# Performance work log

Hardware: AMD Instinct MI355X
Metric: run time of the kernel (lower is better)

The kernel has to match this reference:

```python
import jax, jax.numpy as jnp
import numpy as np

N, M, D = 131072, 2048, 2


def setup_inputs() -> dict:
    key = jax.random.key(0)
    k1, k2 = jax.random.split(key)
    sample = jax.random.normal(k1, (N, D), dtype=jnp.float32)
    mu = jax.random.uniform(k2, (M, D), dtype=jnp.float32)
    # A initialized as 15 * I per component, exactly as in the torch module
    A = (15.0 * jnp.broadcast_to(jnp.eye(D, dtype=jnp.float32), (M, D, D))).astype(jnp.float32)
    w = jnp.ones((M, 1), dtype=jnp.float32)
    return {"sample": sample, "mu": mu, "A": A, "w": w}


def reference(sample, mu, A, w):
    """GaussianMixture.log_likelihoods(sample): logsumexp_j( wlog_j - (x-mu_j)^T G_j (x-mu_j) )."""
    # update_covariances: G_m = A_m A_m^T / 2, shape (M, D, D)
    G = jnp.einsum('mij,mkj->mik', A, A) * 0.5
    g00, g01, g10, g11 = G[:, 0, 0], G[:, 0, 1], G[:, 1, 0], G[:, 1, 1]  # (M,)
    # covariances_determinants (2x2 case) + weights_log
    dets = g00 * g11 - g01 * g10                                          # (M,)
    wlog = jax.nn.log_softmax(w, axis=0)[:, 0] + 0.5 * jnp.log(dets)      # (M,)
    # Pairwise Mahalanobis quadratic form, D=2 expanded to avoid an (N,M,D) temp
    dx0 = sample[:, 0:1] - mu[None, :, 0]   # (N, M)
    dx1 = sample[:, 1:2] - mu[None, :, 1]   # (N, M)
    q = g00 * dx0 * dx0 + (g01 + g10) * dx0 * dx1 + g11 * dx1 * dx1       # (N, M)
    # mode='lse' reduction of kernel_product: log sum_j exp(wlog_j - q_ij)
    ll = jax.nn.logsumexp(wlog[None, :] - q, axis=1, keepdims=True)       # (N, 1)
    return ll
```

## Files before the change

### kernel.cpp

```cpp
#include <hip/hip_runtime.h>
#include <math.h>


#if __has_builtin(__builtin_amdgcn_exp2f)
#define EXP2(x) __builtin_amdgcn_exp2f(x)
#else
#define EXP2(x) exp2f(x)
#endif

typedef float v2f __attribute__((ext_vector_type(2)));

#if __has_builtin(__builtin_elementwise_max)
#define PKMAX(a, b) __builtin_elementwise_max(a, b)
#else
static __device__ inline v2f PKMAX(v2f a, v2f b) {
  v2f r; r.x = fmaxf(a.x, b.x); r.y = fmaxf(a.y, b.y); return r;
}
#endif

#define SPLIT 4
#define YSPLIT 8
#define CH 16

__global__ __launch_bounds__(256) void prep_kernel(
    const float* __restrict__ mu,
    const float* __restrict__ A,
    const float* __restrict__ w,
    float* __restrict__ C,
    int M) {
  __shared__ float red[256];
  const int t = threadIdx.x;

  float mx = -INFINITY;
  for (int m = t; m < M; m += 256) mx = fmaxf(mx, w[m]);
  red[t] = mx; __syncthreads();
  for (int s = 128; s > 0; s >>= 1) {
    if (t < s) red[t] = fmaxf(red[t], red[t + s]);
    __syncthreads();
  }
  const float wmax = red[0]; __syncthreads();

  float sum = 0.f;
  for (int m = t; m < M; m += 256) sum += expf(w[m] - wmax);
  red[t] = sum; __syncthreads();
  for (int s = 128; s > 0; s >>= 1) {
    if (t < s) red[t] += red[t + s];
    __syncthreads();
  }
  const float logZ = wmax + logf(red[0]);

  const float LOG2E = 1.44269504088896340736f;
  const int Ms = M / gridDim.x;
  const int mlo = blockIdx.x * Ms, mhi = mlo + Ms;
  for (int m = mlo + t; m < mhi; m += 256) {
    const float a00 = A[m * 4 + 0], a01 = A[m * 4 + 1];
    const float a10 = A[m * 4 + 2], a11 = A[m * 4 + 3];
    const float g00 = 0.5f * (a00 * a00 + a01 * a01);
    const float g01 = 0.5f * (a00 * a10 + a01 * a11);
    const float g11 = 0.5f * (a10 * a10 + a11 * a11);
    const float g01s = 2.0f * g01;
    const float det = g00 * g11 - g01 * g01;
    const float wlog = (w[m] - logZ) + 0.5f * logf(det);
    const float mu0 = mu[m * 2 + 0], mu1 = mu[m * 2 + 1];
    const float c0 = wlog - (g00 * mu0 * mu0 + g01s * mu0 * mu1 + g11 * mu1 * mu1);
    const float c2 = 2.0f * g00 * mu0 + g01s * mu1;
    const float c4 = 2.0f * g11 * mu1 + g01s * mu0;
    C[0 * M + m] = LOG2E * c0;
    C[1 * M + m] = LOG2E * -g00;
    C[2 * M + m] = LOG2E * c2;
    C[3 * M + m] = LOG2E * -g11;
    C[4 * M + m] = LOG2E * c4;
    C[5 * M + m] = LOG2E * -g01s;
  }

  if (blockIdx.x == 0) {
    __shared__ int uni[256];
    const float r00 = A[0], r01 = A[1], r10 = A[2], r11 = A[3];
    const float rg00 = 0.5f * (r00 * r00 + r01 * r01);
    const float rg01 = 0.5f * (r00 * r10 + r01 * r11);
    const float rg11 = 0.5f * (r10 * r10 + r11 * r11);
    int myuni = 1;
    for (int m = t; m < M; m += 256) {
      const float a00 = A[m * 4 + 0], a01 = A[m * 4 + 1];
      const float a10 = A[m * 4 + 2], a11 = A[m * 4 + 3];
      const float g00 = 0.5f * (a00 * a00 + a01 * a01);
      const float g01 = 0.5f * (a00 * a10 + a01 * a11);
      const float g11 = 0.5f * (a10 * a10 + a11 * a11);
      myuni &= (g00 == rg00) & (g01 == rg01) & (g11 == rg11);
    }
    uni[t] = myuni; __syncthreads();
    for (int s = 128; s > 0; s >>= 1) {
      if (t < s) uni[t] &= uni[t + s];
      __syncthreads();
    }
    if (t == 0) {
      ((int*)C)[6 * M + 0] = uni[0];
      C[6 * M + 1] = LOG2E * -rg00;
      C[6 * M + 2] = LOG2E * -rg11;
      C[6 * M + 3] = LOG2E * -2.0f * rg01;
    }
  }
}

__global__ __launch_bounds__(256) void gmix_kernel(
    const float* __restrict__ sample,
    const float* __restrict__ C,
    float* __restrict__ P,
    int N, int M) {
  __shared__ float Lmx[SPLIT][2][64];
  __shared__ float Lsm[SPLIT][2][64];

  const int lane = threadIdx.x & 63;
  const int wave = __builtin_amdgcn_readfirstlane((int)(threadIdx.x >> 6));
  const int nA = blockIdx.x * 128 + lane;
  const int nB = nA + 64;

  const float2 xA = (nA < N) ? ((const float2*)sample)[nA] : make_float2(0.f, 0.f);
  const float2 xB = (nB < N) ? ((const float2*)sample)[nB] : make_float2(0.f, 0.f);
  const v2f x0p = {xA.x, xB.x};
  const v2f x1p = {xA.y, xB.y};

  const int flag = ((const int*)C)[6 * M + 0];
  const float cb1 = C[6 * M + 1];
  const float cb3 = C[6 * M + 2];
  const float cb5 = C[6 * M + 3];

  const int Mq = M / (SPLIT * YSPLIT);
  const int m0 = (blockIdx.y * SPLIT + wave) * Mq;
  const float* __restrict__ C0 = C + m0;
  const float* __restrict__ C1 = C + M + m0;
  const float* __restrict__ C2 = C + 2 * M + m0;
  const float* __restrict__ C3 = C + 3 * M + m0;
  const float* __restrict__ C4 = C + 4 * M + m0;
  const float* __restrict__ C5 = C + 5 * M + m0;

  v2f basep = {0.f, 0.f};
  float mxA = -INFINITY, sA = 0.0f;
  float mxB = -INFINITY, sB = 0.0f;

  if (flag) {
    basep = cb1 * x0p * x0p + cb3 * x1p * x1p + cb5 * x0p * x1p;
#pragma unroll
    for (int m = 0; m < 64; m += CH) {
      float c0r[CH], c2r[CH], c4r[CH];
#pragma unroll
      for (int j = 0; j < CH; ++j) {
        c0r[j] = C0[m + j]; c2r[j] = C2[m + j]; c4r[j] = C4[m + j];
      }
      v2f a[CH];
#pragma unroll
      for (int j = 0; j < CH; ++j) {
        v2f t = x0p * c2r[j] + c0r[j];
        a[j] = x1p * c4r[j] + t;
      }
      v2f cm01 = PKMAX(a[0], a[1]);
      v2f cm23 = PKMAX(a[2], a[3]);
      v2f cm45 = PKMAX(a[4], a[5]);
      v2f cm67 = PKMAX(a[6], a[7]);
#pragma unroll
      for (int j = 8; j < CH; j += 4) {
        cm01 = PKMAX(cm01, a[j]);
        cm23 = PKMAX(cm23, a[j + 1]);
        cm45 = PKMAX(cm45, a[j + 2]);
        cm67 = PKMAX(cm67, a[j + 3]);
      }
      const v2f cm = PKMAX(PKMAX(cm01, cm23), PKMAX(cm45, cm67));
      const float nmA = fmaxf(mxA, cm.x);
      const float nmB = fmaxf(mxB, cm.y);
      sA *= EXP2(mxA - nmA);
      sB *= EXP2(mxB - nmB);
      const v2f nmp = {nmA, nmB};
      float lA0 = 0.f, lA1 = 0.f, lB0 = 0.f, lB1 = 0.f;
#pragma unroll
      for (int j = 0; j < CH; j += 2) {
        const v2f d0 = a[j] - nmp;
        const v2f d1 = a[j + 1] - nmp;
        lA0 += EXP2(d0.x);
        lB0 += EXP2(d0.y);
        lA1 += EXP2(d1.x);
        lB1 += EXP2(d1.y);
      }
      sA += lA0 + lA1; mxA = nmA;
      sB += lB0 + lB1; mxB = nmB;
    }
  } else {
    for (int m = 0; m < Mq; m += CH) {
      v2f a[CH];
#pragma unroll
      for (int j = 0; j < CH; ++j) {
        const float c0 = C0[m + j], c1 = C1[m + j], c2 = C2[m + j];
        const float c3 = C3[m + j], c4 = C4[m + j], c5 = C5[m + j];
        v2f t0 = x0p * c1 + c2;
        t0 = x1p * c5 + t0;
        v2f t1 = x1p * c3 + c4;
        v2f r = t0 * x0p + c0;
        a[j] = t1 * x1p + r;
      }
      v2f cm01 = PKMAX(a[0], a[1]);
      v2f cm23 = PKMAX(a[2], a[3]);
      v2f cm45 = PKMAX(a[4], a[5]);
      v2f cm67 = PKMAX(a[6], a[7]);
#pragma unroll
      for (int j = 8; j < CH; j += 4) {
        cm01 = PKMAX(cm01, a[j]);
        cm23 = PKMAX(cm23, a[j + 1]);
        cm45 = PKMAX(cm45, a[j + 2]);
        cm67 = PKMAX(cm67, a[j + 3]);
      }
      const v2f cm = PKMAX(PKMAX(cm01, cm23), PKMAX(cm45, cm67));
      const float nmA = fmaxf(mxA, cm.x);
      const float nmB = fmaxf(mxB, cm.y);
      sA *= EXP2(mxA - nmA);
      sB *= EXP2(mxB - nmB);
      const v2f nmp = {nmA, nmB};
      float lA0 = 0.f, lA1 = 0.f, lB0 = 0.f, lB1 = 0.f;
#pragma unroll
      for (int j = 0; j < CH; j += 2) {
        const v2f d0 = a[j] - nmp;
        const v2f d1 = a[j + 1] - nmp;
        lA0 += EXP2(d0.x);
        lB0 += EXP2(d0.y);
        lA1 += EXP2(d1.x);
        lB1 += EXP2(d1.y);
      }
      sA += lA0 + lA1; mxA = nmA;
      sB += lB0 + lB1; mxB = nmB;
    }
  }

  Lmx[wave][0][lane] = mxA + basep.x; Lsm[wave][0][lane] = sA;
  Lmx[wave][1][lane] = mxB + basep.y; Lsm[wave][1][lane] = sB;
  __syncthreads();

  if (wave < 2) {
    const int set = wave;
    const int n = blockIdx.x * 128 + set * 64 + lane;
    if (n < N) {
      float gm = Lmx[0][set][lane];
#pragma unroll
      for (int v = 1; v < SPLIT; ++v) gm = fmaxf(gm, Lmx[v][set][lane]);
      float S = 0.f;
#pragma unroll
      for (int v = 0; v < SPLIT; ++v)
        S += Lsm[v][set][lane] * EXP2(Lmx[v][set][lane] - gm);
      P[blockIdx.y * N + n] = gm + __log2f(S);
    }
  }
}

__global__ __launch_bounds__(256) void combine_kernel(
    const float* __restrict__ P,
    float* __restrict__ out,
    int N) {
  const int n = blockIdx.x * blockDim.x + threadIdx.x;
  if (n >= N) return;
  float p[YSPLIT];
#pragma unroll
  for (int y = 0; y < YSPLIT; ++y) p[y] = P[y * N + n];
  float mx = p[0];
#pragma unroll
  for (int y = 1; y < YSPLIT; ++y) mx = fmaxf(mx, p[y]);
  float S0 = 0.f, S1 = 0.f;
#pragma unroll
  for (int y = 0; y < YSPLIT; y += 2) {
    S0 += EXP2(p[y] - mx);
    S1 += EXP2(p[y + 1] - mx);
  }
  out[n] = (mx + __log2f(S0 + S1)) * 0.69314718055994530942f;
}

extern "C" void kernel_launch(void* const* d_in, const int* in_sizes, int n_in,
                              void* d_out, int out_size, void* d_ws, size_t ws_size,
                              hipStream_t stream) {
  const float* sample = (const float*)d_in[0];
  const float* mu     = (const float*)d_in[1];
  const float* A      = (const float*)d_in[2];
  const float* w      = (const float*)d_in[3];
  float* out = (float*)d_out;

  const int N = in_sizes[0] / 2;
  const int M = in_sizes[3];

  float* C = (float*)d_ws;
  float* P = (float*)d_ws + 6 * M + 16;

  prep_kernel<<<8, 256, 0, stream>>>(mu, A, w, C, M);
  dim3 grid((N + 127) / 128, YSPLIT);
  gmix_kernel<<<grid, 256, 0, stream>>>(sample, C, P, N, M);
  combine_kernel<<<(N + 255) / 256, 256, 0, stream>>>(P, out, N);
}
```

Baseline: 110.5 us.

## Replace online max in logsumexp with precomputed per-sample upper bound shift

Adds a 64x64 grid table of squared nearest-component distances and uses it with the eigenvalue bound of the shared precision to get a per-sample lower bound on the logsumexp maximum. The main loop then sums exp2 directly against this fixed shift, with a clamp to guard overflow. This removes the per-chunk max reduction and rescaling exponentials, and lets the combine stage simply sum partial sums. The cost is an extra table kernel and an extra per-sample buffer. Accuracy depends on the bound staying within the clamp and underflow range, and the path is gated on a new weight-spread check.

Result: slower. 126.6 us (+14.6%).

```diff
diff --git a/kernel.cpp b/kernel.cpp
--- a/kernel.cpp
+++ b/kernel.cpp
@@ -9,18 +9,17 @@
 #endif
 
 typedef float v2f __attribute__((ext_vector_type(2)));
-
-#if __has_builtin(__builtin_elementwise_max)
 #define PKMAX(a, b) __builtin_elementwise_max(a, b)
-#else
-static __device__ inline v2f PKMAX(v2f a, v2f b) {
-  v2f r; r.x = fmaxf(a.x, b.x); r.y = fmaxf(a.y, b.y); return r;
-}
-#endif
+#define PKMIN(a, b) __builtin_elementwise_min(a, b)
 
 #define SPLIT 4
 #define YSPLIT 8
 #define CH 16
+#define GRID 64
+#define NCELL (GRID * GRID)
+#define USHIFT 25.0f
+#define DCLAMP 120.0f
+#define LN2 0.69314718055994530942f
 
 __global__ __launch_bounds__(256) void prep_kernel(
     const float* __restrict__ mu,
@@ -48,6 +47,7 @@
     __syncthreads();
   }
   const float logZ = wmax + logf(red[0]);
+  __syncthreads();
 
   const float LOG2E = 1.44269504088896340736f;
   const int Ms = M / gridDim.x;
@@ -75,11 +75,13 @@
 
   if (blockIdx.x == 0) {
     __shared__ int uni[256];
+    __shared__ float rmin[256], rmax[256];
     const float r00 = A[0], r01 = A[1], r10 = A[2], r11 = A[3];
     const float rg00 = 0.5f * (r00 * r00 + r01 * r01);
     const float rg01 = 0.5f * (r00 * r10 + r01 * r11);
     const float rg11 = 0.5f * (r10 * r10 + r11 * r11);
     int myuni = 1;
+    float wlmin = INFINITY, wlmax = -INFINITY;
     for (int m = t; m < M; m += 256) {
       const float a00 = A[m * 4 + 0], a01 = A[m * 4 + 1];
       const float a10 = A[m * 4 + 2], a11 = A[m * 4 + 3];
@@ -87,28 +89,69 @@
       const float g01 = 0.5f * (a00 * a10 + a01 * a11);
       const float g11 = 0.5f * (a10 * a10 + a11 * a11);
       myuni &= (g00 == rg00) & (g01 == rg01) & (g11 == rg11);
-    }
-    uni[t] = myuni; __syncthreads();
+      const float det = g00 * g11 - g01 * g01;
+      const float wl2 = LOG2E * ((w[m] - logZ) + 0.5f * logf(det));
+      wlmin = fminf(wlmin, wl2);
+      wlmax = fmaxf(wlmax, wl2);
+    }
+    uni[t] = myuni; rmin[t] = wlmin; rmax[t] = wlmax;
+    __syncthreads();
     for (int s = 128; s > 0; s >>= 1) {
-      if (t < s) uni[t] &= uni[t + s];
+      if (t < s) {
+        uni[t] &= uni[t + s];
+        rmin[t] = fminf(rmin[t], rmin[t + s]);
+        rmax[t] = fmaxf(rmax[t], rmax[t + s]);
+      }
       __syncthreads();
     }
     if (t == 0) {
-      ((int*)C)[6 * M + 0] = uni[0];
+      ((int*)C)[6 * M + 0] = uni[0] && ((rmax[0] - rmin[0]) <= 20.0f);
       C[6 * M + 1] = LOG2E * -rg00;
       C[6 * M + 2] = LOG2E * -rg11;
       C[6 * M + 3] = LOG2E * -2.0f * rg01;
-    }
+      C[6 * M + 4] = rmin[0];
+      const float lmax = 0.5f * (rg00 + rg11) +
+                         sqrtf(0.25f * (rg00 - rg11) * (rg00 - rg11) + rg01 * rg01);
+      C[6 * M + 5] = LOG2E * lmax;
+    }
+  }
+}
+
+__global__ __launch_bounds__(256) void table_kernel(
+    const float* __restrict__ mu,
+    float* __restrict__ table,
+    int M) {
+  __shared__ float red[16][17];
+  const int t = threadIdx.x;
+  const int cl = t & 15;
+  const int sl = t >> 4;
+  const int cell = blockIdx.x * 16 + cl;
+  const float cx = ((cell & (GRID - 1)) + 0.5f) * (1.0f / GRID);
+  const float cy = ((cell >> 6) + 0.5f) * (1.0f / GRID);
+  const int per = M / 16;
+  float mn = 1e30f;
+  for (int m = sl * per; m < (sl + 1) * per; ++m) {
+    const float dx = cx - mu[2 * m], dy = cy - mu[2 * m + 1];
+    mn = fminf(mn, fmaf(dx, dx, dy * dy));
+  }
+  red[cl][sl] = mn; __syncthreads();
+  if (sl == 0) {
+    float v = red[cl][0];
+#pragma unroll
+    for (int i = 1; i < 16; ++i) v = fminf(v, red[cl][i]);
+    table[cell] = v;
   }
 }
 
 __global__ __launch_bounds__(256) void gmix_kernel(
     const float* __restrict__ sample,
     const float* __restrict__ C,
+    const float* __restrict__ table,
     float* __restrict__ P,
+    float* __restrict__ Uarr,
     int N, int M) {
+  __shared__ float Lsm[SPLIT][2][64];
   __shared__ float Lmx[SPLIT][2][64];
-  __shared__ float Lsm[SPLIT][2][64];
 
   const int lane = threadIdx.x & 63;
   const int wave = __builtin_amdgcn_readfirstlane((int)(threadIdx.x >> 6));
@@ -134,12 +177,30 @@
   const float* __restrict__ C4 = C + 4 * M + m0;
   const float* __restrict__ C5 = C + 5 * M + m0;
 
-  v2f basep = {0.f, 0.f};
-  float mxA = -INFINITY, sA = 0.0f;
-  float mxB = -INFINITY, sB = 0.0f;
-
   if (flag) {
-    basep = cb1 * x0p * x0p + cb3 * x1p * x1p + cb5 * x0p * x1p;
+    const float wl = C[6 * M + 4];
+    const float lam = C[6 * M + 5];
+    const v2f basep = cb1 * x0p * x0p + cb3 * x1p * x1p + cb5 * x0p * x1p;
+
+    float Uf[2];
+#pragma unroll
+    for (int k = 0; k < 2; ++k) {
+      const float sx0 = (k == 0) ? xA.x : xB.x;
+      const float sx1 = (k == 0) ? xA.y : xB.y;
+      const float px = fminf(fmaxf(sx0, 0.f), 1.f);
+      const float py = fminf(fmaxf(sx1, 0.f), 1.f);
+      const int ix = (int)fminf(px * GRID, GRID - 1.0f);
+      const int iy = (int)fminf(py * GRID, GRID - 1.0f);
+      const float dc = sqrtf(table[iy * GRID + ix]);
+      const float dx = sx0 - px, dy = sx1 - py;
+      const float rr = sqrtf(fmaf(dx, dx, dy * dy));
+      const float D = rr + dc + 0.012f;
+      Uf[k] = wl - lam * D * D + USHIFT;
+    }
+    const v2f V = {Uf[0] - basep.x, Uf[1] - basep.y};
+    const v2f dcl = {DCLAMP, DCLAMP};
+
+    v2f acc0 = {0.f, 0.f}, acc1 = {0.f, 0.f}, acc2 = {0.f, 0.f}, acc3 = {0.f, 0.f};
 #pragma unroll
     for (int m = 0; m < 64; m += CH) {
       float c0r[CH], c2r[CH], c4r[CH];
@@ -147,43 +208,41 @@
       for (int j = 0; j < CH; ++j) {
         c0r[j] = C0[m + j]; c2r[j] = C2[m + j]; c4r[j] = C4[m + j];
       }
-      v2f a[CH];
 #pragma unroll
       for (int j = 0; j < CH; ++j) {
-        v2f t = x0p * c2r[j] + c0r[j];
-        a[j] = x1p * c4r[j] + t;
-      }
-      v2f cm01 = PKMAX(a[0], a[1]);
-      v2f cm23 = PKMAX(a[2], a[3]);
-      v2f cm45 = PKMAX(a[4], a[5]);
-      v2f cm67 = PKMAX(a[6], a[7]);
-#pragma unroll
-      for (int j = 8; j < CH; j += 4) {
-        cm01 = PKMAX(cm01, a[j]);
-        cm23 = PKMAX(cm23, a[j + 1]);
-        cm45 = PKMAX(cm45, a[j + 2]);
-        cm67 = PKMAX(cm67, a[j + 3]);
-      }
-      const v2f cm = PKMAX(PKMAX(cm01, cm23), PKMAX(cm45, cm67));
-      const float nmA = fmaxf(mxA, cm.x);
-      const float nmB = fmaxf(mxB, cm.y);
-      sA *= EXP2(mxA - nmA);
-      sB *= EXP2(mxB - nmB);
-      const v2f nmp = {nmA, nmB};
-      float lA0 = 0.f, lA1 = 0.f, lB0 = 0.f, lB1 = 0.f;
-#pragma unroll
-      for (int j = 0; j < CH; j += 2) {
-        const v2f d0 = a[j] - nmp;
-        const v2f d1 = a[j + 1] - nmp;
-        lA0 += EXP2(d0.x);
-        lB0 += EXP2(d0.y);
-        lA1 += EXP2(d1.x);
-        lB1 += EXP2(d1.y);
-      }
-      sA += lA0 + lA1; mxA = nmA;
-      sB += lB0 + lB1; mxB = nmB;
+        const v2f t = x0p * c2r[j] + c0r[j];
+        const v2f a = x1p * c4r[j] + t;
+        const v2f d = PKMIN(a - V, dcl);
+        v2f e;
+        e.x = EXP2(d.x);
+        e.y = EXP2(d.y);
+        if ((j & 3) == 0) acc0 += e;
+        else if ((j & 3) == 1) acc1 += e;
+        else if ((j & 3) == 2) acc2 += e;
+        else acc3 += e;
+      }
+    }
+    const v2f S2 = (acc0 + acc1) + (acc2 + acc3);
+
+    Lsm[wave][0][lane] = S2.x;
+    Lsm[wave][1][lane] = S2.y;
+    __syncthreads();
+
+    if (wave < 2) {
+      const int set = wave;
+      const int n = blockIdx.x * 128 + set * 64 + lane;
+      if (n < N) {
+        float S = Lsm[0][set][lane];
+#pragma unroll
+        for (int v = 1; v < SPLIT; ++v) S += Lsm[v][set][lane];
+        P[blockIdx.y * N + n] = S;
+        if (blockIdx.y == 0) Uarr[n] = Uf[set];
+      }
     }
   } else {
+    v2f basep = cb1 * x0p * x0p + cb3 * x1p * x1p + cb5 * x0p * x1p;
+    float mxA = -INFINITY, sA = 0.0f;
+    float mxB = -INFINITY, sB = 0.0f;
     for (int m = 0; m < Mq; m += CH) {
       v2f a[CH];
 #pragma unroll
@@ -226,47 +285,55 @@
       sA += lA0 + lA1; mxA = nmA;
       sB += lB0 + lB1; mxB = nmB;
     }
-  }
-
-  Lmx[wave][0][lane] = mxA + basep.x; Lsm[wave][0][lane] = sA;
-  Lmx[wave][1][lane] = mxB + basep.y; Lsm[wave][1][lane] = sB;
-  __syncthreads();
-
-  if (wave < 2) {
-    const int set = wave;
-    const int n = blockIdx.x * 128 + set * 64 + lane;
-    if (n < N) {
-      float gm = Lmx[0][set][lane];
-#pragma unroll
-      for (int v = 1; v < SPLIT; ++v) gm = fmaxf(gm, Lmx[v][set][lane]);
-      float S = 0.f;
-#pragma unroll
-      for (int v = 0; v < SPLIT; ++v)
-        S += Lsm[v][set][lane] * EXP2(Lmx[v][set][lane] - gm);
-      P[blockIdx.y * N + n] = gm + __log2f(S);
+    Lmx[wave][0][lane] = mxA + basep.x; Lsm[wave][0][lane] = sA;
+    Lmx[wave][1][lane] = mxB + basep.y; Lsm[wave][1][lane] = sB;
+    __syncthreads();
+    if (wave < 2) {
+      const int set = wave;
+      const int n = blockIdx.x * 128 + set * 64 + lane;
+      if (n < N) {
+        float gm = Lmx[0][set][lane];
+#pragma unroll
+        for (int v = 1; v < SPLIT; ++v) gm = fmaxf(gm, Lmx[v][set][lane]);
+        float S = 0.f;
+#pragma unroll
+        for (int v = 0; v < SPLIT; ++v)
+          S += Lsm[v][set][lane] * EXP2(Lmx[v][set][lane] - gm);
+        P[blockIdx.y * N + n] = gm + __log2f(S);
+      }
     }
   }
 }
 
 __global__ __launch_bounds__(256) void combine_kernel(
     const float* __restrict__ P,
+    const float* __restrict__ Uarr,
+    const float* __restrict__ C,
     float* __restrict__ out,
-    int N) {
+    int N, int M) {
   const int n = blockIdx.x * blockDim.x + threadIdx.x;
   if (n >= N) return;
-  float p[YSPLIT];
-#pragma unroll
-  for (int y = 0; y < YSPLIT; ++y) p[y] = P[y * N + n];
-  float mx = p[0];
-#pragma unroll
-  for (int y = 1; y < YSPLIT; ++y) mx = fmaxf(mx, p[y]);
-  float S0 = 0.f, S1 = 0.f;
-#pragma unroll
-  for (int y = 0; y < YSPLIT; y += 2) {
-    S0 += EXP2(p[y] - mx);
-    S1 += EXP2(p[y + 1] - mx);
-  }
-  out[n] = (mx + __log2f(S0 + S1)) * 0.69314718055994530942f;
+  const int flag = ((const int*)C)[6 * M + 0];
+  if (flag) {
+    float S = 0.f;
+#pragma unroll
+    for (int y = 0; y < YSPLIT; ++y) S += P[y * N + n];
+    out[n] = (Uarr[n] + __log2f(S)) * LN2;
+  } else {
+    float p[YSPLIT];
+#pragma unroll
+    for (int y = 0; y < YSPLIT; ++y) p[y] = P[y * N + n];
+    float mx = p[0];
+#pragma unroll
+    for (int y = 1; y < YSPLIT; ++y) mx = fmaxf(mx, p[y]);
+    float S0 = 0.f, S1 = 0.f;
+#pragma unroll
+    for (int y = 0; y < YSPLIT; y += 2) {
+      S0 += EXP2(p[y] - mx);
+      S1 += EXP2(p[y + 1] - mx);
+    }
+    out[n] = (mx + __log2f(S0 + S1)) * LN2;
+  }
 }
 
 extern "C" void kernel_launch(void* const* d_in, const int* in_sizes, int n_in,
@@ -281,11 +348,14 @@
   const int N = in_sizes[0] / 2;
   const int M = in_sizes[3];
 
-  float* C = (float*)d_ws;
-  float* P = (float*)d_ws + 6 * M + 16;
+  float* C     = (float*)d_ws;
+  float* table = C + 6 * M + 16;
+  float* P     = table + NCELL;
+  float* Uarr  = P + YSPLIT * N;
 
   prep_kernel<<<8, 256, 0, stream>>>(mu, A, w, C, M);
+  table_kernel<<<NCELL / 16, 256, 0, stream>>>(mu, table, M);
   dim3 grid((N + 127) / 128, YSPLIT);
-  gmix_kernel<<<grid, 256, 0, stream>>>(sample, C, P, N, M);
-  combine_kernel<<<(N + 255) / 256, 256, 0, stream>>>(P, out, N);
-}
+  gmix_kernel<<<grid, 256, 0, stream>>>(sample, C, table, P, Uarr, N, M);
+  combine_kernel<<<(N + 255) / 256, 256, 0, stream>>>(P, Uarr, C, out, N, M);
+}
```
